# Kernel optimization log

Measured on AMD Instinct MI355X. Metric: run time of the kernel, lower is better.

Reference implementation:

```python
import jax, jax.numpy as jnp
import numpy as np

def binarize(t):
    # deterministic sign binarization to {-1, +1}
    return jnp.where(t >= 0, 1.0, -1.0).astype(t.dtype)

def setup_inputs() -> dict:
    key = jax.random.key(0)
    k1, k2 = jax.random.split(key)
    x = jax.random.normal(k1, (8192, 4096), dtype=jnp.float32)
    kernel = jax.random.normal(k2, (4096, 4096), dtype=jnp.float32)
    return {"x": x, "kernel": kernel}

def reference(x, kernel):
    # BinaryLayer.call with binary=True: matmul(binarize(x), binarize(W))
    return jnp.matmul(binarize(x), binarize(kernel))
```

## Files before the change

kernel.cpp:

```cpp
#include <hip/hip_runtime.h>
#include <stdint.h>

#define MDIM 8192
#define NDIM 4096
#define KDIM 4096
#define NT   (KDIM / 128)
#define TILEB 16384

#define BM 256
#define BN 256
#define BUFSZ 32768

typedef __attribute__((ext_vector_type(4)))  int   i32x4;
typedef __attribute__((ext_vector_type(8)))  int   i32x8;
typedef __attribute__((ext_vector_type(16))) float f32x16;

__device__ __forceinline__ void gload16(const void* g, void* l) {
    __builtin_amdgcn_global_load_lds(
        (const __attribute__((address_space(1))) void*)g,
        (__attribute__((address_space(3))) void*)l, 16, 0, 0);
}

__device__ __forceinline__ i32x8 pad8(i32x4 v) {
    i32x8 r;
    r[0] = v[0]; r[1] = v[1]; r[2] = v[2]; r[3] = v[3];
    r[4] = 0;    r[5] = 0;    r[6] = 0;    r[7] = 0;
    return r;
}

#define MFMA_FP4_32(a, b, c)                                                 \
    __builtin_amdgcn_mfma_scale_f32_32x32x64_f8f6f4(                          \
        (a), (b), (c), 4, 4, 0, 0x7F7F7F7F, 0, 0x7F7F7F7F)

__global__ __launch_bounds__(256) void pack_a4_kernel(const float* __restrict__ X,
                                                      uint8_t* __restrict__ A4p) {
    int tg    = blockIdx.x * 256 + threadIdx.x;
    int row   = tg & 255;
    int slot  = (tg >> 8) & 3;
    int kt    = (tg >> 10) & 31;
    int panel = tg >> 15;
    const float4* src = (const float4*)(X + (size_t)(panel * 256 + row) * KDIM
                                          + kt * 128 + slot * 32);
    uint32_t w[4];
#pragma unroll
    for (int q = 0; q < 4; ++q) {
        float4 a = src[q * 2], b = src[q * 2 + 1];
        w[q] = (a.x >= 0.f ? 0x2u : 0xAu)        | ((a.y >= 0.f ? 0x2u : 0xAu) << 4)
             | ((a.z >= 0.f ? 0x2u : 0xAu) << 8) | ((a.w >= 0.f ? 0x2u : 0xAu) << 12)
             | ((b.x >= 0.f ? 0x2u : 0xAu) << 16)| ((b.y >= 0.f ? 0x2u : 0xAu) << 20)
             | ((b.z >= 0.f ? 0x2u : 0xAu) << 24)| ((b.w >= 0.f ? 0x2u : 0xAu) << 28);
    }
    ((uint4*)A4p)[tg] = make_uint4(w[0], w[1], w[2], w[3]);
}

__global__ __launch_bounds__(256) void pack_b4t_kernel(const float* __restrict__ W,
                                                       uint8_t* __restrict__ B4p) {
    __shared__ uint8_t P[64 * 80];
    const int t  = threadIdx.x;
    const int n0 = blockIdx.x * 64;
    const int k0 = blockIdx.y * 128;
    const int nt = t & 15, ks = t >> 4;
    uint32_t a0 = 0, a1 = 0, a2 = 0, a3 = 0;
#pragma unroll
    for (int j = 0; j < 8; ++j) {
        float4 v = *(const float4*)&W[(size_t)(k0 + ks * 8 + j) * NDIM + n0 + nt * 4];
        int sh = (j >> 1) * 8 + (j & 1) * 4;
        a0 |= (v.x >= 0.f ? 0x2u : 0xAu) << sh;
        a1 |= (v.y >= 0.f ? 0x2u : 0xAu) << sh;
        a2 |= (v.z >= 0.f ? 0x2u : 0xAu) << sh;
        a3 |= (v.w >= 0.f ? 0x2u : 0xAu) << sh;
    }
    *(uint32_t*)&P[(nt * 4 + 0) * 80 + ks * 4] = a0;
    *(uint32_t*)&P[(nt * 4 + 1) * 80 + ks * 4] = a1;
    *(uint32_t*)&P[(nt * 4 + 2) * 80 + ks * 4] = a2;
    *(uint32_t*)&P[(nt * 4 + 3) * 80 + ks * 4] = a3;
    __syncthreads();
    const int n = t >> 2, slot = t & 3;
    uint4 val = *(const uint4*)&P[n * 80 + slot * 16];
    const int pn = (n0 + n) >> 8, rn = (n0 + n) & 255;
    size_t addr = ((((size_t)pn * 32 + blockIdx.y) * 4 + slot) * 256 + rn) * 16;
    *(uint4*)&B4p[addr] = val;
}

__global__ __launch_bounds__(512, 2) void binmm_fp4_kernel(const uint8_t* __restrict__ A4p,
                                                           const uint8_t* __restrict__ B4p,
                                                           float* __restrict__ C) {
    __shared__ uint8_t lds[4 * BUFSZ];

    const int tid = threadIdx.x, lane = tid & 63, wid = tid >> 6;
    const int wr = wid >> 2, wc = wid & 3;
    const int l31 = lane & 31, kh = lane >> 5;
    const int m0 = blockIdx.y * BM, n0 = blockIdx.x * BN;

    const uint8_t* pA = A4p + (size_t)blockIdx.y * 32 * TILEB + tid * 16;
    const uint8_t* pB = B4p + (size_t)blockIdx.x * 32 * TILEB + tid * 16;

#define STAGE(bufOff, t) do {                                                  \
        gload16(pA + (t) * TILEB,        lds + (bufOff) + tid * 16);           \
        gload16(pA + (t) * TILEB + 8192, lds + (bufOff) + 8192  + tid * 16);   \
        gload16(pB + (t) * TILEB,        lds + (bufOff) + 16384 + tid * 16);   \
        gload16(pB + (t) * TILEB + 8192, lds + (bufOff) + 24576 + tid * 16);   \
    } while (0)

    const int aBase = kh * 4096 + (wr * 128 + l31) * 16;
    const int bBase = 16384 + kh * 4096 + (wc * 64 + l31) * 16;

    f32x16 acc[4][2];
#pragma unroll
    for (int m = 0; m < 4; ++m)
#pragma unroll
        for (int n = 0; n < 2; ++n)
#pragma unroll
            for (int e = 0; e < 16; ++e) acc[m][n][e] = 0.f;

#define COMPUTE(bufOff) do {                                                   \
        const uint8_t* bp_ = lds + (bufOff);                                   \
        i32x8 bF[2][2];                                                        \
        _Pragma("unroll")                                                      \
        for (int nf = 0; nf < 2; ++nf)                                         \
            _Pragma("unroll")                                                  \
            for (int s = 0; s < 2; ++s)                                        \
                bF[nf][s] = pad8(*(const i32x4*)(bp_ + bBase + nf * 512 + s * 8192)); \
        __builtin_amdgcn_s_setprio(1);                                         \
        _Pragma("unroll")                                                      \
        for (int s = 0; s < 2; ++s)                                            \
            _Pragma("unroll")                                                  \
            for (int mf = 0; mf < 4; ++mf) {                                   \
                i32x8 a8 = pad8(*(const i32x4*)(bp_ + aBase + mf * 512 + s * 8192)); \
                acc[mf][0] = MFMA_FP4_32(a8, bF[0][s], acc[mf][0]);            \
                acc[mf][1] = MFMA_FP4_32(a8, bF[1][s], acc[mf][1]);            \
            }                                                                  \
        __builtin_amdgcn_s_setprio(0);                                         \
    } while (0)

#define SYNC(n) do {                                                           \
        __builtin_amdgcn_sched_barrier(0);                                     \
        asm volatile("s_waitcnt vmcnt(" #n ")" ::: "memory");                  \
        __builtin_amdgcn_s_barrier();                                          \
        __builtin_amdgcn_sched_barrier(0);                                     \
    } while (0)

    STAGE(0, 0);
    STAGE(BUFSZ, 1);
    STAGE(2 * BUFSZ, 2);
    SYNC(8);

#pragma unroll 1
    for (int t = 0; t < NT - 3; ++t) {
        STAGE(((t + 3) & 3) * BUFSZ, t + 3);
        COMPUTE((t & 3) * BUFSZ);
        SYNC(8);
    }
    COMPUTE(1 * BUFSZ);
    SYNC(4);
    COMPUTE(2 * BUFSZ);
    SYNC(0);
    COMPUTE(3 * BUFSZ);

#pragma unroll
    for (int mf = 0; mf < 4; ++mf) {
#pragma unroll
        for (int nf = 0; nf < 2; ++nf) {
            size_t cc = (size_t)(n0 + wc * 64 + nf * 32 + l31);
            int rbase = m0 + wr * 128 + mf * 32 + 4 * kh;
#pragma unroll
            for (int reg = 0; reg < 16; ++reg) {
                int rr = (reg & 3) + 8 * (reg >> 2);
                C[(size_t)(rbase + rr) * NDIM + cc] = acc[mf][nf][reg];
            }
        }
    }
#undef STAGE
#undef COMPUTE
#undef SYNC
}

extern "C" void kernel_launch(void* const* d_in, const int* in_sizes, int n_in,
                              void* d_out, int out_size, void* d_ws, size_t ws_size,
                              hipStream_t stream) {
    const float* x = (const float*)d_in[0];
    const float* w = (const float*)d_in[1];
    float* out = (float*)d_out;

    uint8_t* A4p = (uint8_t*)d_ws;
    uint8_t* B4p = (uint8_t*)d_ws + (size_t)MDIM * (KDIM / 2);

    pack_a4_kernel<<<(int)((size_t)MDIM * KDIM / 32 / 256), 256, 0, stream>>>(x, A4p);
    pack_b4t_kernel<<<dim3(NDIM / 64, KDIM / 128), 256, 0, stream>>>(w, B4p);
    binmm_fp4_kernel<<<dim3(NDIM / BN, MDIM / BM), 512, 0, stream>>>(A4p, B4p, out);
}
```

Measured before the change: 135.5 us.

## Use 1024-thread GEMM blocks with smaller per-wave tiles and coalesce A packing

The GEMM block goes from 8 to 16 waves. Each wave now owns a 64x64 output tile with a 2x2 accumulator set, and each thread issues half as many global-to-LDS loads per stage, with the vmcnt waits adjusted to match. Separately, the A-packing kernel is remapped so each wave reads contiguous row data from X and scatters into the same packed layout, which should coalesce the fp32 reads. More waves can hide latency better, but each wave has less register reuse, does more LDS reads per MFMA, and makes barriers costlier. The launch bound of 1024 threads with 4 blocks per CU is also unlikely to be achievable given the 128KB LDS per block.

```diff
diff --git a/kernel.cpp b/kernel.cpp
--- a/kernel.cpp
+++ b/kernel.cpp
@@ -34,13 +34,11 @@
 
 __global__ __launch_bounds__(256) void pack_a4_kernel(const float* __restrict__ X,
                                                       uint8_t* __restrict__ A4p) {
-    int tg    = blockIdx.x * 256 + threadIdx.x;
-    int row   = tg & 255;
-    int slot  = (tg >> 8) & 3;
-    int kt    = (tg >> 10) & 31;
-    int panel = tg >> 15;
-    const float4* src = (const float4*)(X + (size_t)(panel * 256 + row) * KDIM
-                                          + kt * 128 + slot * 32);
+    int gw   = blockIdx.x * 4 + (threadIdx.x >> 6);
+    int lane = threadIdx.x & 63;
+    int row  = gw >> 1, chunk = gw & 1;
+    const float4* src = (const float4*)(X + (size_t)row * KDIM
+                                          + chunk * 2048 + lane * 32);
     uint32_t w[4];
 #pragma unroll
     for (int q = 0; q < 4; ++q) {
@@ -50,7 +48,9 @@
              | ((b.x >= 0.f ? 0x2u : 0xAu) << 16)| ((b.y >= 0.f ? 0x2u : 0xAu) << 20)
              | ((b.z >= 0.f ? 0x2u : 0xAu) << 24)| ((b.w >= 0.f ? 0x2u : 0xAu) << 28);
     }
-    ((uint4*)A4p)[tg] = make_uint4(w[0], w[1], w[2], w[3]);
+    int kt = chunk * 16 + (lane >> 2), slot = lane & 3;
+    size_t unit = ((((size_t)(row >> 8) * 32 + kt) * 4 + slot) * 256) + (row & 255);
+    ((uint4*)A4p)[unit] = make_uint4(w[0], w[1], w[2], w[3]);
 }
 
 __global__ __launch_bounds__(256) void pack_b4t_kernel(const float* __restrict__ W,
@@ -82,9 +82,9 @@
     *(uint4*)&B4p[addr] = val;
 }
 
-__global__ __launch_bounds__(512, 2) void binmm_fp4_kernel(const uint8_t* __restrict__ A4p,
-                                                           const uint8_t* __restrict__ B4p,
-                                                           float* __restrict__ C) {
+__global__ __launch_bounds__(1024, 4) void binmm_fp4_kernel(const uint8_t* __restrict__ A4p,
+                                                            const uint8_t* __restrict__ B4p,
+                                                            float* __restrict__ C) {
     __shared__ uint8_t lds[4 * BUFSZ];
 
     const int tid = threadIdx.x, lane = tid & 63, wid = tid >> 6;
@@ -96,18 +96,16 @@
     const uint8_t* pB = B4p + (size_t)blockIdx.x * 32 * TILEB + tid * 16;
 
 #define STAGE(bufOff, t) do {                                                  \
-        gload16(pA + (t) * TILEB,        lds + (bufOff) + tid * 16);           \
-        gload16(pA + (t) * TILEB + 8192, lds + (bufOff) + 8192  + tid * 16);   \
-        gload16(pB + (t) * TILEB,        lds + (bufOff) + 16384 + tid * 16);   \
-        gload16(pB + (t) * TILEB + 8192, lds + (bufOff) + 24576 + tid * 16);   \
+        gload16(pA + (t) * TILEB, lds + (bufOff) + tid * 16);                  \
+        gload16(pB + (t) * TILEB, lds + (bufOff) + 16384 + tid * 16);          \
     } while (0)
 
-    const int aBase = kh * 4096 + (wr * 128 + l31) * 16;
+    const int aBase = kh * 4096 + (wr * 64 + l31) * 16;
     const int bBase = 16384 + kh * 4096 + (wc * 64 + l31) * 16;
 
-    f32x16 acc[4][2];
+    f32x16 acc[2][2];
 #pragma unroll
-    for (int m = 0; m < 4; ++m)
+    for (int m = 0; m < 2; ++m)
 #pragma unroll
         for (int n = 0; n < 2; ++n)
 #pragma unroll
@@ -115,22 +113,19 @@
 
 #define COMPUTE(bufOff) do {                                                   \
         const uint8_t* bp_ = lds + (bufOff);                                   \
-        i32x8 bF[2][2];                                                        \
         _Pragma("unroll")                                                      \
-        for (int nf = 0; nf < 2; ++nf)                                         \
-            _Pragma("unroll")                                                  \
-            for (int s = 0; s < 2; ++s)                                        \
-                bF[nf][s] = pad8(*(const i32x4*)(bp_ + bBase + nf * 512 + s * 8192)); \
-        __builtin_amdgcn_s_setprio(1);                                         \
-        _Pragma("unroll")                                                      \
-        for (int s = 0; s < 2; ++s)                                            \
-            _Pragma("unroll")                                                  \
-            for (int mf = 0; mf < 4; ++mf) {                                   \
-                i32x8 a8 = pad8(*(const i32x4*)(bp_ + aBase + mf * 512 + s * 8192)); \
-                acc[mf][0] = MFMA_FP4_32(a8, bF[0][s], acc[mf][0]);            \
-                acc[mf][1] = MFMA_FP4_32(a8, bF[1][s], acc[mf][1]);            \
-            }                                                                  \
-        __builtin_amdgcn_s_setprio(0);                                         \
+        for (int s = 0; s < 2; ++s) {                                          \
+            i32x4 a0 = *(const i32x4*)(bp_ + aBase + s * 8192);                \
+            i32x4 a1 = *(const i32x4*)(bp_ + aBase + 512 + s * 8192);          \
+            i32x4 b0 = *(const i32x4*)(bp_ + bBase + s * 8192);                \
+            i32x4 b1 = *(const i32x4*)(bp_ + bBase + 512 + s * 8192);          \
+            __builtin_amdgcn_s_setprio(1);                                     \
+            acc[0][0] = MFMA_FP4_32(pad8(a0), pad8(b0), acc[0][0]);            \
+            acc[0][1] = MFMA_FP4_32(pad8(a0), pad8(b1), acc[0][1]);            \
+            acc[1][0] = MFMA_FP4_32(pad8(a1), pad8(b0), acc[1][0]);            \
+            acc[1][1] = MFMA_FP4_32(pad8(a1), pad8(b1), acc[1][1]);            \
+            __builtin_amdgcn_s_setprio(0);                                     \
+        }                                                                      \
     } while (0)
 
 #define SYNC(n) do {                                                           \
@@ -143,26 +138,26 @@
     STAGE(0, 0);
     STAGE(BUFSZ, 1);
     STAGE(2 * BUFSZ, 2);
-    SYNC(8);
+    SYNC(4);
 
 #pragma unroll 1
     for (int t = 0; t < NT - 3; ++t) {
         STAGE(((t + 3) & 3) * BUFSZ, t + 3);
         COMPUTE((t & 3) * BUFSZ);
-        SYNC(8);
+        SYNC(4);
     }
     COMPUTE(1 * BUFSZ);
-    SYNC(4);
+    SYNC(2);
     COMPUTE(2 * BUFSZ);
     SYNC(0);
     COMPUTE(3 * BUFSZ);
 
 #pragma unroll
-    for (int mf = 0; mf < 4; ++mf) {
+    for (int mf = 0; mf < 2; ++mf) {
 #pragma unroll
         for (int nf = 0; nf < 2; ++nf) {
             size_t cc = (size_t)(n0 + wc * 64 + nf * 32 + l31);
-            int rbase = m0 + wr * 128 + mf * 32 + 4 * kh;
+            int rbase = m0 + wr * 64 + mf * 32 + 4 * kh;
 #pragma unroll
             for (int reg = 0; reg < 16; ++reg) {
                 int rr = (reg & 3) + 8 * (reg >> 2);
@@ -185,7 +180,7 @@
     uint8_t* A4p = (uint8_t*)d_ws;
     uint8_t* B4p = (uint8_t*)d_ws + (size_t)MDIM * (KDIM / 2);
 
-    pack_a4_kernel<<<(int)((size_t)MDIM * KDIM / 32 / 256), 256, 0, stream>>>(x, A4p);
+    pack_a4_kernel<<<MDIM * 2 / 4, 256, 0, stream>>>(x, A4p);
     pack_b4t_kernel<<<dim3(NDIM / 64, KDIM / 128), 256, 0, stream>>>(w, B4p);
-    binmm_fp4_kernel<<<dim3(NDIM / BN, MDIM / BM), 512, 0, stream>>>(A4p, B4p, out);
+    binmm_fp4_kernel<<<dim3(NDIM / BN, MDIM / BM), 1024, 0, stream>>>(A4p, B4p, out);
 }
```

Result: no change. 135.4 us (-0.1%).
